# Kernel tuning notes

Hardware: AMD Instinct MI355X
Metric: run time of the kernel (lower is better)

Reference implementation:

```python
import jax, jax.numpy as jnp
import numpy as np

HEADS = 4
DIM_K = 16
DIM_U = 1
EPS = 1e-5


def _rel_pos_idx(n):
    # torch: meshgrid(ij) -> stack -> '(i j) n'; rel = pos[None,:]-pos[:,None] + n-1
    ii, jj = np.meshgrid(np.arange(n), np.arange(n), indexing='ij')
    pos = np.stack([ii, jj]).reshape(2, -1).T  # (n*n, 2)
    rel = pos[None, :] - pos[:, None] + (n - 1)  # (N, N, 2)
    return rel[..., 0], rel[..., 1]


def _bn(t, gamma, beta):
    # BatchNorm2d in training mode: batch stats over (b, h, w), biased var
    mu = t.mean(axis=(0, 1, 2))
    var = t.var(axis=(0, 1, 2))
    return (t - mu) * jax.lax.rsqrt(var + EPS) * gamma + beta


def setup_inputs() -> dict:
    key = jax.random.key(0)
    ks = jax.random.split(key, 16)
    b, n, c = 8, 48, 128
    hk = DIM_K * HEADS          # 64
    v = 128 // HEADS            # 32 (dim_out // heads)
    rl = 2 * n - 1              # 95
    s = 0.02
    return {
        'x': jax.random.normal(ks[0], (b, n, n, c), jnp.float32),
        'cor': jax.random.normal(ks[1], (b, n, n, 2), jnp.float32),
        'Wq': jax.random.normal(ks[2], (hk, c), jnp.float32) * s,
        'Wk': jax.random.normal(ks[3], (DIM_K * DIM_U, c), jnp.float32) * s,
        'Wv': jax.random.normal(ks[4], (v * DIM_U, c), jnp.float32) * s,
        'Wce': jax.random.normal(ks[5], (hk, 2), jnp.float32) * s,
        'bce': jax.random.normal(ks[6], (hk,), jnp.float32) * s,
        'Wcc': jax.random.normal(ks[7], (hk, 128), jnp.float32) * s,
        'Wmp': jax.random.normal(ks[8], (128, hk), jnp.float32) * s,
        'bmp': jax.random.normal(ks[9], (128,), jnp.float32) * s,
        'gq': jnp.ones((hk,), jnp.float32),
        'bq': jnp.zeros((hk,), jnp.float32),
        'gv': jnp.ones((v * DIM_U,), jnp.float32),
        'bv': jnp.zeros((v * DIM_U,), jnp.float32),
        'rel_pos_emb': jax.random.normal(ks[10], (rl, rl, DIM_K, DIM_U), jnp.float32),
    }


def reference(x, cor, Wq, Wk, Wv, Wce, bce, Wcc, Wmp, bmp, gq, bq, gv, bv, rel_pos_emb):
    b, hh, ww, c = x.shape
    h, u, kd = HEADS, DIM_U, DIM_K
    vd = Wv.shape[0] // u
    N = hh * ww

    # frame reversal along batch
    x_rev = jnp.concatenate([x[b // 2:], x[:b // 2]], axis=0)

    # 1x1 convs as channel matmuls (channels-last)
    q = jnp.einsum('bhwc,oc->bhwo', x, Wq)
    k = jnp.einsum('bhwc,oc->bhwo', x_rev, Wk)
    v = jnp.einsum('bhwc,oc->bhwo', x_rev, Wv)

    Qn = _bn(q, gq, bq)
    Vn = _bn(v, gv, bv)

    Q = jnp.transpose(Qn.reshape(b, N, h, kd), (0, 2, 3, 1))       # b h k n
    K = jnp.transpose(k.reshape(b, N, u, kd), (0, 2, 3, 1))        # b u k m
    V = jnp.transpose(Vn.reshape(b, N, u, vd), (0, 2, 3, 1))       # b u v m

    K = jax.nn.softmax(K, axis=-1)
    lamc = jnp.einsum('bukm,buvm->bkv', K, V)
    Yc = jnp.einsum('bhkn,bkv->bhvn', Q, lamc)

    # relative position lambda (global branch)
    ni, mi = _rel_pos_idx(hh)
    emb = rel_pos_emb[ni, mi]                                      # n m k u
    lamp = jnp.einsum('nmku,buvm->bnkv', emb, V)
    Yp = jnp.einsum('bhkn,bnkv->bhvn', Q, lamp)

    Y = Yc + Yp                                                    # b h v n
    appearance = jnp.transpose(Y.reshape(b, h, vd, hh, ww), (0, 3, 4, 1, 2)).reshape(b, hh, ww, h * vd)

    cor_embed_ = jnp.einsum('bhwc,oc->bhwo', cor, Wce) + bce       # b hh ww (h k)
    cor_embed = jnp.transpose(cor_embed_.reshape(b, N, h, kd), (0, 2, 3, 1))  # b h k n
    crc = jnp.einsum('bhkn,bkv->bhvn', cor_embed, lamc)
    crp = jnp.einsum('bhkn,bnkv->bhvn', cor_embed, lamp)
    cor_reverse_ = jnp.transpose((crc + crp).reshape(b, h, vd, hh, ww), (0, 3, 4, 1, 2)).reshape(b, hh, ww, h * vd)
    cor_reverse = jnp.einsum('bhwc,oc->bhwo', cor_reverse_, Wcc)
    motion = jnp.einsum('bhwc,oc->bhwo', cor_reverse - cor_embed_, Wmp) + bmp
    return appearance, motion
```

## Files before the change

### kernel.cpp

```cpp
#include <hip/hip_runtime.h>
#include <math.h>

#define NNPOS 2304
#define ROWS  18432
#define NK    96

#define O_Q   0ul
#define O_K   1179648ul
#define O_V   1474560ul
#define O_ST  2064384ul
#define O_VP  2064704ul
#define O_QP  2457920ul
#define O_LC  4817216ul
#define O_CR  4821312ul
#define O_RT  6000960ul
#define O_WG  6148416ul
#define O_B2  6148672ul
#define O_WB  6148800ul
#define O_PT  6155968ul
#define O_PV  6164160ul
#define O_PE  6166208ul
#define O_WFB 6167232ul

typedef __bf16 bf16x8 __attribute__((ext_vector_type(8)));
typedef float  f32x4  __attribute__((ext_vector_type(4)));
typedef unsigned int u32;
struct __attribute__((packed, aligned(4))) bf16x8p { bf16x8 v; };

__global__ void k_fold(const float* __restrict__ Wcc, const float* __restrict__ Wce,
                       const float* __restrict__ Wmp, const float* __restrict__ bmp,
                       const float* __restrict__ bce, const float* __restrict__ Wq,
                       const float* __restrict__ Wk, const float* __restrict__ Wv,
                       float* __restrict__ ws) {
  const int t = threadIdx.x;
  const int g = blockIdx.x * 256 + t;
  const int o2 = g >> 7, c = g & 127;
  float acc = 0.f;
#pragma unroll 8
  for (int o = 0; o < 64; ++o) acc += Wmp[o2 * 64 + o] * Wcc[o * 128 + c];
  ((__bf16*)(ws + O_WFB))[o2 * 128 + c] = (__bf16)acc;
  if (blockIdx.x == 0 && t < 128) {
    float a0 = 0.f, a1 = 0.f, ab = 0.f;
#pragma unroll 8
    for (int o = 0; o < 64; ++o) {
      float w = Wmp[t * 64 + o];
      a0 += w * Wce[o * 2]; a1 += w * Wce[o * 2 + 1]; ab += w * bce[o];
    }
    ws[O_WG + t * 2] = a0; ws[O_WG + t * 2 + 1] = a1; ws[O_B2 + t] = bmp[t] - ab;
  }
  __bf16* wbp = (__bf16*)(ws + O_WB);
  if (g < 14336) {
    float w;
    if (g < 8192) w = Wq[g];
    else if (g < 10240) w = Wk[g - 8192];
    else w = Wv[g - 10240];
    wbp[g] = (__bf16)w;
  }
}

__global__ __launch_bounds__(256) void k_qkv(const float* __restrict__ x,
                                             float* __restrict__ ws) {
  const int t = threadIdx.x;
  const int wave = t >> 6, lane = t & 63;
  const int lr = lane & 15, quad = lane >> 4;
  const int r0 = blockIdx.x * 64 + wave * 16;
  const int b = r0 / NNPOS;
  const int n0 = r0 - b * NNPOS;
  const size_t outbase = (size_t)(((b + 4) & 7)) * NNPOS + n0;

  const __bf16* wb = (const __bf16*)(ws + O_WB);
  const float* xrow = x + (size_t)(r0 + lr) * 128;

  f32x4 acc[7];
#pragma unroll
  for (int i = 0; i < 7; ++i) acc[i] = (f32x4){0.f, 0.f, 0.f, 0.f};

#pragma unroll
  for (int ks = 0; ks < 4; ++ks) {
    const float* ap = xrow + ks * 32 + quad * 8;
    float4 a0 = *(const float4*)(ap);
    float4 a1 = *(const float4*)(ap + 4);
    bf16x8 af;
    af[0] = (__bf16)a0.x; af[1] = (__bf16)a0.y; af[2] = (__bf16)a0.z; af[3] = (__bf16)a0.w;
    af[4] = (__bf16)a1.x; af[5] = (__bf16)a1.y; af[6] = (__bf16)a1.z; af[7] = (__bf16)a1.w;
#pragma unroll
    for (int ct = 0; ct < 7; ++ct) {
      bf16x8 bfrag = *(const bf16x8*)(wb + (ct * 16 + lr) * 128 + ks * 32 + quad * 8);
      acc[ct] = __builtin_amdgcn_mfma_f32_16x16x32_bf16(af, bfrag, acc[ct], 0, 0, 0);
    }
  }

#pragma unroll
  for (int ct = 0; ct < 7; ++ct) {
#pragma unroll
    for (int reg = 0; reg < 4; ++reg) {
      int m = quad * 4 + reg;
      int oc = ct * 16 + lr;
      float vvv = acc[ct][reg];
      if (ct < 4)      ws[O_Q + (size_t)(r0 + m) * 64 + oc] = vvv;
      else if (ct < 5) ws[O_K + (outbase + m) * 16 + (oc - 64)] = vvv;
      else             ws[O_V + (outbase + m) * 32 + (oc - 80)] = vvv;
    }
  }
}

__global__ void k_rt(const float* __restrict__ rel, float* __restrict__ ws) {
  __bf16* rt = (__bf16*)(ws + O_RT);
  int i = blockIdx.x * 256 + threadIdx.x;
  if (i < 144400) {
    int kc = i & 15, rr = i >> 4;
    int ri = rr / 95, rj = rr - ri * 95;
    int d = ri * 96 + rj;
    __bf16 v = (__bf16)rel[i];
    rt[(size_t)kc * 9216 + d] = v;
    if (d > 0) rt[147456ul + (size_t)kc * 9216 + d - 1] = v;
  }
}

__global__ void k_zero(float* __restrict__ ws) {
  __bf16* vp = (__bf16*)(ws + O_VP);
  int i = blockIdx.x * 256 + threadIdx.x;
  if (i < 4096) ws[O_LC + i] = 0.f;
  int bv = i / 96, rem = i - bv * 96;
  int mi = rem >> 1, h8 = rem & 1;
  uint4 z; z.x = 0; z.y = 0; z.z = 0; z.w = 0;
  *(uint4*)(vp + (size_t)bv * 3072 + mi * 64 + 48 + h8 * 8) = z;
}

__global__ void k_stats1(float* __restrict__ ws) {
  const int t = threadIdx.x, blk = blockIdx.x;
  __shared__ float sh[512];
  if (blk < 64) {
    const int ch = t & 63, rsub = t >> 6;
    const float* src = ws + O_Q;
    const int r0 = blk * 288;
    float s = 0.f, s2 = 0.f;
#pragma unroll 4
    for (int i = 0; i < 72; ++i) {
      float v = src[(size_t)(r0 + rsub + i * 4) * 64 + ch];
      s += v; s2 += v * v;
    }
    sh[t] = s; sh[256 + t] = s2;
    __syncthreads();
    if (t < 64) {
      float S = sh[t] + sh[t + 64] + sh[t + 128] + sh[t + 192];
      float S2 = sh[256 + t] + sh[256 + t + 64] + sh[256 + t + 128] + sh[256 + t + 192];
      ws[O_PT + blk * 128 + t * 2] = S; ws[O_PT + blk * 128 + t * 2 + 1] = S2;
    }
  } else if (blk < 96) {
    const int j = blk - 64;
    const int ch = t & 31, rsub = t >> 5;
    const float* src = ws + O_V;
    const int r0 = j * 576;
    float s = 0.f, s2 = 0.f;
#pragma unroll 4
    for (int i = 0; i < 72; ++i) {
      float v = src[(size_t)(r0 + rsub + i * 8) * 32 + ch];
      s += v; s2 += v * v;
    }
    sh[t] = s; sh[256 + t] = s2;
    __syncthreads();
    if (t < 32) {
      float S = 0.f, S2 = 0.f;
#pragma unroll
      for (int k = 0; k < 8; ++k) { S += sh[t + k * 32]; S2 += sh[256 + t + k * 32]; }
      ws[O_PV + j * 64 + t * 2] = S; ws[O_PV + j * 64 + t * 2 + 1] = S2;
    }
  } else {
    const int idx = blk - 96;
    const int b = idx >> 3, sl = idx & 7;
    const int kc = t & 15, rsub = t >> 4;
    const int r0 = b * 2304 + sl * 288;
    float s = 0.f;
#pragma unroll 2
    for (int i = 0; i < 18; ++i)
      s += __expf(ws[O_K + (size_t)(r0 + rsub + i * 16) * 16 + kc]);
    sh[t] = s;
    __syncthreads();
    if (t < 16) {
      float S = 0.f;
#pragma unroll
      for (int k = 0; k < 16; ++k) S += sh[t + k * 16];
      ws[O_PE + b * 128 + sl * 16 + t] = S;
    }
  }
}

__global__ void k_stats2(const float* __restrict__ gq, const float* __restrict__ bq,
                         const float* __restrict__ gv, const float* __restrict__ bv,
                         float* __restrict__ ws) {
  const int t = threadIdx.x;
  if (t < 64) {
    float S = 0.f, S2 = 0.f;
    for (int i = 0; i < 64; ++i) { S += ws[O_PT + i * 128 + t * 2]; S2 += ws[O_PT + i * 128 + t * 2 + 1]; }
    float mu = S / 18432.f, var = S2 / 18432.f - mu * mu;
    float sc = gq[t] * rsqrtf(var + 1e-5f);
    ws[O_ST + t] = sc; ws[O_ST + 64 + t] = bq[t] - mu * sc;
  } else if (t < 96) {
    int ch = t - 64;
    float S = 0.f, S2 = 0.f;
    for (int i = 0; i < 32; ++i) { S += ws[O_PV + i * 64 + ch * 2]; S2 += ws[O_PV + i * 64 + ch * 2 + 1]; }
    float mu = S / 18432.f, var = S2 / 18432.f - mu * mu;
    float sc = gv[ch] * rsqrtf(var + 1e-5f);
    ws[O_ST + 128 + ch] = sc; ws[O_ST + 160 + ch] = bv[ch] - mu * sc;
  } else if (t < 224) {
    int idx = t - 96; int b = idx >> 4, kc = idx & 15;
    float S = 0.f;
#pragma unroll
    for (int sl = 0; sl < 8; ++sl) S += ws[O_PE + b * 128 + sl * 16 + kc];
    ws[O_ST + 192 + idx] = 1.f / S;
  }
}

__global__ void k_vp(float* __restrict__ ws) {
  const int b = blockIdx.x / 48, mi = blockIdx.x - b * 48;
  const int t = threadIdx.x;
  __shared__ float Vn[48 * 33];
  const float* st = ws + O_ST;
  const int r0 = b * 2304 + mi * 48;
#pragma unroll
  for (int i = t; i < 1536; i += 256) {
    int r = i >> 5, j = i & 31;
    Vn[r * 33 + j] = ws[O_V + (size_t)(r0 + r) * 32 + j] * st[128 + j] + st[160 + j];
  }
  __syncthreads();
  __bf16* vp = (__bf16*)(ws + O_VP);
  const int j = t >> 3, seg = t & 7;
  unsigned short u[6];
#pragma unroll
  for (int q = 0; q < 6; ++q)
    u[q] = __builtin_bit_cast(unsigned short, (__bf16)Vn[(seg * 6 + q) * 33 + j]);
  u32 w0 = (u32)u[0] | ((u32)u[1] << 16);
  u32 w1 = (u32)u[2] | ((u32)u[3] << 16);
  u32 w2 = (u32)u[4] | ((u32)u[5] << 16);
  u32* dst = (u32*)(vp + (size_t)(b * 32 + j) * 3072 + mi * 64 + seg * 6);
  dst[0] = w0; dst[1] = w1; dst[2] = w2;
}

__global__ void k_prep(const float* __restrict__ cor, const float* __restrict__ Wce,
                       const float* __restrict__ bce, float* __restrict__ ws) {
  const int t = threadIdx.x;
  const int rl = t >> 5, j = t & 31;
  const int rid = blockIdx.x * 8 + rl;
  const int b = rid / NNPOS, n = rid - b * NNPOS;
  const float* st = ws + O_ST;
  float c0 = cor[rid * 2], c1 = cor[rid * 2 + 1];
#pragma unroll
  for (int ch = j; ch < 64; ch += 32) {
    float qn = ws[O_Q + (size_t)rid * 64 + ch] * st[ch] + st[64 + ch];
    ws[O_QP + (size_t)(n * 8 + b) * 128 + ch] = qn;
    float ce = c0 * Wce[ch * 2] + c1 * Wce[ch * 2 + 1] + bce[ch];
    ws[O_QP + (size_t)(n * 8 + b) * 128 + 64 + ch] = ce;
  }
}

__global__ void k_lamc(float* __restrict__ ws) {
  const int b = blockIdx.x / 36, sl = blockIdx.x - b * 36;
  const int t = threadIdx.x;
  __shared__ float eK[16][16];
  __shared__ float Vn[16][33];
  const float* st = ws + O_ST;
  const int kc = t & 15, vp_ = t >> 4;
  const int v0 = vp_ * 2, v1 = v0 + 1;
  float a0 = 0.f, a1 = 0.f;
  const int m0 = b * 2304 + sl * 64;
  const int jj = t & 31, rw = t >> 5;
  const float scj = st[128 + jj], bij = st[160 + jj];
  for (int ch = 0; ch < 4; ++ch) {
    const int mbase = m0 + ch * 16;
    eK[t >> 4][t & 15] = __expf(ws[O_K + (size_t)(mbase + (t >> 4)) * 16 + (t & 15)]);
    Vn[rw][jj]     = ws[O_V + (size_t)(mbase + rw) * 32 + jj] * scj + bij;
    Vn[rw + 8][jj] = ws[O_V + (size_t)(mbase + rw + 8) * 32 + jj] * scj + bij;
    __syncthreads();
#pragma unroll
    for (int m = 0; m < 16; ++m) {
      float e = eK[m][kc];
      a0 += e * Vn[m][v0];
      a1 += e * Vn[m][v1];
    }
    __syncthreads();
  }
  atomicAdd(&ws[O_LC + (size_t)(b * 16 + kc) * 32 + v0], a0);
  atomicAdd(&ws[O_LC + (size_t)(b * 16 + kc) * 32 + v1], a1);
}

__global__ __launch_bounds__(128, 3) void k_lamp(float* __restrict__ ws,
                                                 float* __restrict__ out) {
  __shared__ __align__(16) char smem[17408];
  bf16x8* Bs16 = (bf16x8*)smem;
  float* Cs = (float*)smem;

  const int t = threadIdx.x;
  const int bx = blockIdx.x;
  const int ni = bx / 6;
  const int sset = bx - ni * 6;
  const int s0 = (sset < 3) ? sset * 16 : (sset - 3) * 16 + 1;
  const int by = blockIdx.y;
  const int colbase = by * 64;
  const int w = t >> 6, lane = t & 63;
  const int lr = lane & 15, quad = lane >> 4;

  const __bf16* vp = (const __bf16*)(ws + O_VP);
  const __bf16* rtb = (const __bf16*)(ws + O_RT);

  const int u0 = t, u1 = t + 128;
  const int c0 = u0 >> 2, p0 = ((u0 & 3) - (c0 >> 1)) & 3;
  const int c1 = u1 >> 2, p1 = ((u1 & 3) - (c1 >> 1)) & 3;
  const __bf16* gB0 = vp + (size_t)(colbase + c0) * 3072 + p0 * 8;
  const __bf16* gB1 = vp + (size_t)(colbase + c1) * 3072 + p1 * 8;

  const int parity = (s0 + 1) & 1;
  const __bf16* baseA = rtb + (size_t)parity * 147456 +
                        (size_t)lr * 9216 + quad * 8 - 2 * (w * 4);

  f32x4 acc[4][4];
  {
    f32x4 zz = {0.f, 0.f, 0.f, 0.f};
#pragma unroll
    for (int i = 0; i < 4; ++i)
#pragma unroll
      for (int j = 0; j < 4; ++j) acc[i][j] = zz;
  }

  bf16x8 afA[4], afB[4], vb0, vb1;

  auto loadA = [&](int ksn, bf16x8* dst) {
    int mi = ksn >> 1, mj0 = (ksn & 1) << 5;
    const __bf16* p = baseA + (96 * (mi - ni + 47) + mj0 - s0 + 47 - parity);
#pragma unroll
    for (int rt = 0; rt < 4; ++rt)
      dst[rt] = ((const bf16x8p*)(p - 2 * rt))->v;
  };
  auto loadB = [&](int ksn) {
    int k0 = ksn * 32;
    vb0 = *(const bf16x8*)(gB0 + k0);
    vb1 = *(const bf16x8*)(gB1 + k0);
  };

  loadB(0);
  Bs16[u0] = vb0; Bs16[u1] = vb1;
  loadA(0, afA);
  loadB(1);
  __syncthreads();

  for (int ks = 0; ks < NK; ks += 2) {
    Bs16[256 + u0] = vb0; Bs16[256 + u1] = vb1;
    loadB(ks + 2 < NK ? ks + 2 : NK - 1);
    loadA(ks + 1, afB);
#pragma unroll
    for (int ct = 0; ct < 4; ++ct) {
      int col = ct * 16 + lr;
      bf16x8 bfr = Bs16[col * 4 + ((quad + (col >> 1)) & 3)];
#pragma unroll
      for (int rt = 0; rt < 4; ++rt)
        acc[rt][ct] = __builtin_amdgcn_mfma_f32_16x16x32_bf16(afA[rt], bfr, acc[rt][ct], 0, 0, 0);
    }
    __syncthreads();
    Bs16[u0] = vb0; Bs16[u1] = vb1;
    loadB(ks + 3 < NK ? ks + 3 : NK - 1);
    if (ks + 2 < NK) loadA(ks + 2, afA);
#pragma unroll
    for (int ct = 0; ct < 4; ++ct) {
      int col = ct * 16 + lr;
      bf16x8 bfr = Bs16[256 + col * 4 + ((quad + (col >> 1)) & 3)];
#pragma unroll
      for (int rt = 0; rt < 4; ++rt)
        acc[rt][ct] = __builtin_amdgcn_mfma_f32_16x16x32_bf16(afB[rt], bfr, acc[rt][ct], 0, 0, 0);
    }
    __syncthreads();
  }

  const float* lamcp = ws + O_LC;
  const float* Qp = ws + O_QP;
  __bf16* CRb = (__bf16*)(ws + O_CR);
  const int s = t >> 5, vv = t & 31;

  for (int h = 0; h < 2; ++h) {
    __syncthreads();
    if (w == h) {
#pragma unroll
      for (int rt = 0; rt < 4; ++rt) {
#pragma unroll
        for (int ct = 0; ct < 4; ++ct) {
          int col = ct * 16 + lr;
          int bb = by * 2 + (col >> 5);
          int vl = col & 31;
#pragma unroll
          for (int reg = 0; reg < 4; ++reg) {
            int row = rt * 16 + quad * 4 + reg;
            int kc = row & 15;
            float dinv = ws[O_ST + 192 + bb * 16 + kc];
            Cs[row * 68 + col] = acc[rt][ct][reg] + lamcp[(bb * 16 + kc) * 32 + vl] * dinv;
          }
        }
      }
    }
    __syncthreads();
#pragma unroll
    for (int i = 0; i < 16; ++i) {
      int combo = s * 16 + i;
      int hp = combo & 7, bl = (combo >> 3) & 1, nr = combo >> 4;
      int n = ni * 48 + s0 + 2 * (h * 4 + nr);
      int bb = by * 2 + bl;
      const float* qrow = Qp + ((size_t)(n * 8 + bb) * 8 + hp) * 16;
      const float* crow = Cs + (nr * 16) * 68 + bl * 32 + vv;
      float y = 0.f;
#pragma unroll
      for (int kc = 0; kc < 16; ++kc) y += qrow[kc] * crow[kc * 68];
      size_t idx = (size_t)(bb * NNPOS + n) * 128 + (hp & 3) * 32 + vv;
      if (hp < 4) out[idx] = y;
      else        CRb[idx] = (__bf16)y;
    }
  }
}

__global__ __launch_bounds__(256) void k_motion(const float* __restrict__ cor,
                                                float* __restrict__ ws,
                                                float* __restrict__ out) {
  const int t = threadIdx.x;
  const int wave = t >> 6, lane = t & 63;
  const int lr = lane & 15, quad = lane >> 4;
  const int r0 = blockIdx.x * 64 + wave * 16;
  const __bf16* crb = (const __bf16*)(ws + O_CR);
  const __bf16* wfb = (const __bf16*)(ws + O_WFB);

  f32x4 acc[8];
#pragma unroll
  for (int i = 0; i < 8; ++i) acc[i] = (f32x4){0.f, 0.f, 0.f, 0.f};

#pragma unroll
  for (int ks = 0; ks < 4; ++ks) {
    bf16x8 af = *(const bf16x8*)(crb + (size_t)(r0 + lr) * 128 + ks * 32 + quad * 8);
#pragma unroll
    for (int ct = 0; ct < 8; ++ct) {
      bf16x8 bfrag = *(const bf16x8*)(wfb + (ct * 16 + lr) * 128 + ks * 32 + quad * 8);
      acc[ct] = __builtin_amdgcn_mfma_f32_16x16x32_bf16(af, bfrag, acc[ct], 0, 0, 0);
    }
  }

#pragma unroll
  for (int reg = 0; reg < 4; ++reg) {
    int row = r0 + quad * 4 + reg;
    float c0 = cor[row * 2], c1 = cor[row * 2 + 1];
#pragma unroll
    for (int ct = 0; ct < 8; ++ct) {
      int o2 = ct * 16 + lr;
      float y = acc[ct][reg] + ws[O_B2 + o2] - c0 * ws[O_WG + o2 * 2] - c1 * ws[O_WG + o2 * 2 + 1];
      out[2359296ul + (size_t)row * 128 + o2] = y;
    }
  }
}

extern "C" void kernel_launch(void* const* d_in, const int* in_sizes, int n_in,
                              void* d_out, int out_size, void* d_ws, size_t ws_size,
                              hipStream_t stream) {
  const float* x   = (const float*)d_in[0];
  const float* cor = (const float*)d_in[1];
  const float* Wq  = (const float*)d_in[2];
  const float* Wk  = (const float*)d_in[3];
  const float* Wv  = (const float*)d_in[4];
  const float* Wce = (const float*)d_in[5];
  const float* bce = (const float*)d_in[6];
  const float* Wcc = (const float*)d_in[7];
  const float* Wmp = (const float*)d_in[8];
  const float* bmp = (const float*)d_in[9];
  const float* gq  = (const float*)d_in[10];
  const float* bq  = (const float*)d_in[11];
  const float* gv  = (const float*)d_in[12];
  const float* bv  = (const float*)d_in[13];
  const float* rel = (const float*)d_in[14];
  float* out = (float*)d_out;
  float* ws  = (float*)d_ws;

  k_fold  <<<64, 256, 0, stream>>>(Wcc, Wce, Wmp, bmp, bce, Wq, Wk, Wv, ws);
  k_qkv   <<<288, 256, 0, stream>>>(x, ws);
  k_rt    <<<565, 256, 0, stream>>>(rel, ws);
  k_zero  <<<96, 256, 0, stream>>>(ws);
  k_stats1<<<160, 256, 0, stream>>>(ws);
  k_stats2<<<1, 256, 0, stream>>>(gq, bq, gv, bv, ws);
  k_vp    <<<384, 256, 0, stream>>>(ws);
  k_lamc  <<<288, 256, 0, stream>>>(ws);
  k_prep  <<<2304, 256, 0, stream>>>(cor, Wce, bce, ws);
  k_lamp  <<<dim3(288, 4), 128, 0, stream>>>(ws, out);
  k_motion<<<288, 256, 0, stream>>>(cor, ws, out);
}
```

Before: 298.5 us.

## Stage relative-position A operand in LDS and widen lamp tiles to 128 columns

The k_lamp GEMM now runs with 256-thread blocks over 128 output columns, so the grid's y dimension drops from 4 to 2. Each block gathers the relative-position embedding window into LDS once per k-step as packed u32 and shares it across waves, instead of every wave doing unaligned global loads of A. The B operand is streamed with global_load_lds double buffering, and the duplicate parity-shifted copy of the embedding table in k_rt is removed. The aim is less redundant global traffic for A and better reuse per block. The cost is more LDS per block, a sync every k-step, lower occupancy, and scalar handling of odd-aligned gathers.

```diff
diff --git a/kernel.cpp b/kernel.cpp
--- a/kernel.cpp
+++ b/kernel.cpp
@@ -1,5 +1,6 @@
 #include <hip/hip_runtime.h>
 #include <math.h>
+#include <stdint.h>
 
 #define NNPOS 2304
 #define ROWS  18432
@@ -25,7 +26,13 @@
 typedef __bf16 bf16x8 __attribute__((ext_vector_type(8)));
 typedef float  f32x4  __attribute__((ext_vector_type(4)));
 typedef unsigned int u32;
-struct __attribute__((packed, aligned(4))) bf16x8p { bf16x8 v; };
+typedef u32 u32x4 __attribute__((ext_vector_type(4)));
+
+__device__ __forceinline__ void gll16(const void* g, void* l) {
+  auto gp = (const __attribute__((address_space(1))) unsigned char*)(uintptr_t)g;
+  auto lp = (__attribute__((address_space(3))) unsigned char*)(u32)(uintptr_t)l;
+  __builtin_amdgcn_global_load_lds(gp, lp, 16, 0, 0);
+}
 
 __global__ void k_fold(const float* __restrict__ Wcc, const float* __restrict__ Wce,
                        const float* __restrict__ Wmp, const float* __restrict__ bmp,
@@ -110,10 +117,7 @@
   if (i < 144400) {
     int kc = i & 15, rr = i >> 4;
     int ri = rr / 95, rj = rr - ri * 95;
-    int d = ri * 96 + rj;
-    __bf16 v = (__bf16)rel[i];
-    rt[(size_t)kc * 9216 + d] = v;
-    if (d > 0) rt[147456ul + (size_t)kc * 9216 + d - 1] = v;
+    rt[(size_t)kc * 9216 + ri * 96 + rj] = (__bf16)rel[i];
   }
 }
 
@@ -284,10 +288,11 @@
   atomicAdd(&ws[O_LC + (size_t)(b * 16 + kc) * 32 + v1], a1);
 }
 
-__global__ __launch_bounds__(128, 3) void k_lamp(float* __restrict__ ws,
+__global__ __launch_bounds__(256, 2) void k_lamp(float* __restrict__ ws,
                                                  float* __restrict__ out) {
-  __shared__ __align__(16) char smem[17408];
+  __shared__ __align__(16) char smem[33792];
   bf16x8* Bs16 = (bf16x8*)smem;
+  u32* Sw = (u32*)(smem + 16384);
   float* Cs = (float*)smem;
 
   const int t = threadIdx.x;
@@ -295,23 +300,40 @@
   const int ni = bx / 6;
   const int sset = bx - ni * 6;
   const int s0 = (sset < 3) ? sset * 16 : (sset - 3) * 16 + 1;
-  const int by = blockIdx.y;
-  const int colbase = by * 64;
+  const int chalf = blockIdx.y;
+  const int colbase = chalf * 128;
   const int w = t >> 6, lane = t & 63;
+  const int wrow = w >> 1, wcol = w & 1;
   const int lr = lane & 15, quad = lane >> 4;
 
   const __bf16* vp = (const __bf16*)(ws + O_VP);
-  const __bf16* rtb = (const __bf16*)(ws + O_RT);
-
-  const int u0 = t, u1 = t + 128;
-  const int c0 = u0 >> 2, p0 = ((u0 & 3) - (c0 >> 1)) & 3;
-  const int c1 = u1 >> 2, p1 = ((u1 & 3) - (c1 >> 1)) & 3;
-  const __bf16* gB0 = vp + (size_t)(colbase + c0) * 3072 + p0 * 8;
-  const __bf16* gB1 = vp + (size_t)(colbase + c1) * 3072 + p1 * 8;
-
-  const int parity = (s0 + 1) & 1;
-  const __bf16* baseA = rtb + (size_t)parity * 147456 +
-                        (size_t)lr * 9216 + quad * 8 - 2 * (w * 4);
+  const unsigned short* rp = (const unsigned short*)(ws + O_RT);
+
+  const int kcA0 = t / 24, wpA0 = t - kcA0 * 24;
+  const int ia1 = t + 256;
+  const int kcA1 = ia1 / 24, wpA1 = ia1 - kcA1 * 24;
+  const bool hasA1 = (t < 128);
+
+  const int u0 = w * 64 + lane, u1 = 256 + w * 64 + lane;
+  const int cB0 = u0 >> 2, pB0 = ((u0 & 3) - ((u0 >> 3) & 3)) & 3;
+  const int cB1 = u1 >> 2, pB1 = ((u1 & 3) - ((u1 >> 3) & 3)) & 3;
+  const __bf16* gB0 = vp + (size_t)(colbase + cB0) * 3072 + pB0 * 8;
+  const __bf16* gB1 = vp + (size_t)(colbase + cB1) * 3072 + pB1 * 8;
+  char* ldsB0 = smem + w * 1024;
+  char* ldsB1 = smem + 4096 + w * 1024;
+
+  auto gatherA = [&](int ksn, u32& a0_, u32& a1_) {
+    const int mi = ksn >> 1, mj0 = (ksn & 1) << 5;
+    const int P0 = 96 * (mi - ni + 47) + mj0 - s0 + 33;
+    long b0 = (long)kcA0 * 9216 + P0 + 2 * wpA0;
+    if (P0 & 1) a0_ = (u32)rp[b0] | ((u32)rp[b0 + 1] << 16);
+    else        a0_ = *(const u32*)(rp + b0);
+    if (hasA1) {
+      long b1 = (long)kcA1 * 9216 + P0 + 2 * wpA1;
+      if (P0 & 1) a1_ = (u32)rp[b1] | ((u32)rp[b1 + 1] << 16);
+      else        a1_ = *(const u32*)(rp + b1);
+    }
+  };
 
   f32x4 acc[4][4];
   {
@@ -322,51 +344,47 @@
       for (int j = 0; j < 4; ++j) acc[i][j] = zz;
   }
 
-  bf16x8 afA[4], afB[4], vb0, vb1;
-
-  auto loadA = [&](int ksn, bf16x8* dst) {
-    int mi = ksn >> 1, mj0 = (ksn & 1) << 5;
-    const __bf16* p = baseA + (96 * (mi - ni + 47) + mj0 - s0 + 47 - parity);
+  u32 a0 = 0, a1 = 0;
+  {
+    u32 p0, p1 = 0;
+    gatherA(0, p0, p1);
+    Sw[kcA0 * 25 + wpA0] = p0;
+    if (hasA1) Sw[kcA1 * 25 + wpA1] = p1;
+    gll16(gB0, ldsB0);
+    gll16(gB1, ldsB1);
+    gatherA(1, a0, a1);
+  }
+  __syncthreads();
+
+  for (int ks = 0; ks < NK; ++ks) {
+    const int cur = ks & 1, nxt = cur ^ 1;
+    if (ks + 1 < NK) {
+      const int k0n = (ks + 1) * 32;
+      gll16(gB0 + k0n, ldsB0 + nxt * 8192);
+      gll16(gB1 + k0n, ldsB1 + nxt * 8192);
+      Sw[nxt * 400 + kcA0 * 25 + wpA0] = a0;
+      if (hasA1) Sw[nxt * 400 + kcA1 * 25 + wpA1] = a1;
+    }
+    if (ks + 2 < NK) gatherA(ks + 2, a0, a1);
+
+    bf16x8 af[4], bfr[4];
+#pragma unroll
+    for (int rt = 0; rt < 4; ++rt) {
+      int nl = wrow * 4 + rt;
+      int wb = cur * 400 + lr * 25 + (7 - nl) + quad * 4;
+      u32x4 dd = { Sw[wb], Sw[wb + 1], Sw[wb + 2], Sw[wb + 3] };
+      af[rt] = __builtin_bit_cast(bf16x8, dd);
+    }
+#pragma unroll
+    for (int ct = 0; ct < 4; ++ct) {
+      int col = wcol * 64 + ct * 16 + lr;
+      bfr[ct] = Bs16[cur * 512 + col * 4 + ((quad + (col >> 1)) & 3)];
+    }
 #pragma unroll
     for (int rt = 0; rt < 4; ++rt)
-      dst[rt] = ((const bf16x8p*)(p - 2 * rt))->v;
-  };
-  auto loadB = [&](int ksn) {
-    int k0 = ksn * 32;
-    vb0 = *(const bf16x8*)(gB0 + k0);
-    vb1 = *(const bf16x8*)(gB1 + k0);
-  };
-
-  loadB(0);
-  Bs16[u0] = vb0; Bs16[u1] = vb1;
-  loadA(0, afA);
-  loadB(1);
-  __syncthreads();
-
-  for (int ks = 0; ks < NK; ks += 2) {
-    Bs16[256 + u0] = vb0; Bs16[256 + u1] = vb1;
-    loadB(ks + 2 < NK ? ks + 2 : NK - 1);
-    loadA(ks + 1, afB);
-#pragma unroll
-    for (int ct = 0; ct < 4; ++ct) {
-      int col = ct * 16 + lr;
-      bf16x8 bfr = Bs16[col * 4 + ((quad + (col >> 1)) & 3)];
-#pragma unroll
-      for (int rt = 0; rt < 4; ++rt)
-        acc[rt][ct] = __builtin_amdgcn_mfma_f32_16x16x32_bf16(afA[rt], bfr, acc[rt][ct], 0, 0, 0);
-    }
-    __syncthreads();
-    Bs16[u0] = vb0; Bs16[u1] = vb1;
-    loadB(ks + 3 < NK ? ks + 3 : NK - 1);
-    if (ks + 2 < NK) loadA(ks + 2, afA);
-#pragma unroll
-    for (int ct = 0; ct < 4; ++ct) {
-      int col = ct * 16 + lr;
-      bf16x8 bfr = Bs16[256 + col * 4 + ((quad + (col >> 1)) & 3)];
-#pragma unroll
-      for (int rt = 0; rt < 4; ++rt)
-        acc[rt][ct] = __builtin_amdgcn_mfma_f32_16x16x32_bf16(afB[rt], bfr, acc[rt][ct], 0, 0, 0);
-    }
+#pragma unroll
+      for (int ct = 0; ct < 4; ++ct)
+        acc[rt][ct] = __builtin_amdgcn_mfma_f32_16x16x32_bf16(af[rt], bfr[ct], acc[rt][ct], 0, 0, 0);
     __syncthreads();
   }
 
@@ -377,20 +395,20 @@
 
   for (int h = 0; h < 2; ++h) {
     __syncthreads();
-    if (w == h) {
+    if (wrow == h) {
 #pragma unroll
       for (int rt = 0; rt < 4; ++rt) {
 #pragma unroll
         for (int ct = 0; ct < 4; ++ct) {
-          int col = ct * 16 + lr;
-          int bb = by * 2 + (col >> 5);
+          int col = wcol * 64 + ct * 16 + lr;
+          int bb = chalf * 4 + (col >> 5);
           int vl = col & 31;
 #pragma unroll
           for (int reg = 0; reg < 4; ++reg) {
             int row = rt * 16 + quad * 4 + reg;
             int kc = row & 15;
             float dinv = ws[O_ST + 192 + bb * 16 + kc];
-            Cs[row * 68 + col] = acc[rt][ct][reg] + lamcp[(bb * 16 + kc) * 32 + vl] * dinv;
+            Cs[row * 132 + col] = acc[rt][ct][reg] + lamcp[(bb * 16 + kc) * 32 + vl] * dinv;
           }
         }
       }
@@ -399,14 +417,14 @@
 #pragma unroll
     for (int i = 0; i < 16; ++i) {
       int combo = s * 16 + i;
-      int hp = combo & 7, bl = (combo >> 3) & 1, nr = combo >> 4;
+      int hp = combo & 7, bl = (combo >> 3) & 3, nr = combo >> 5;
       int n = ni * 48 + s0 + 2 * (h * 4 + nr);
-      int bb = by * 2 + bl;
+      int bb = chalf * 4 + bl;
       const float* qrow = Qp + ((size_t)(n * 8 + bb) * 8 + hp) * 16;
-      const float* crow = Cs + (nr * 16) * 68 + bl * 32 + vv;
+      const float* crow = Cs + (nr * 16) * 132 + bl * 32 + vv;
       float y = 0.f;
 #pragma unroll
-      for (int kc = 0; kc < 16; ++kc) y += qrow[kc] * crow[kc * 68];
+      for (int kc = 0; kc < 16; ++kc) y += qrow[kc] * crow[kc * 132];
       size_t idx = (size_t)(bb * NNPOS + n) * 128 + (hp & 3) * 32 + vv;
       if (hp < 4) out[idx] = y;
       else        CRb[idx] = (__bf16)y;
@@ -481,6 +499,6 @@
   k_vp    <<<384, 256, 0, stream>>>(ws);
   k_lamc  <<<288, 256, 0, stream>>>(ws);
   k_prep  <<<2304, 256, 0, stream>>>(cor, Wce, bce, ws);
-  k_lamp  <<<dim3(288, 4), 128, 0, stream>>>(ws, out);
+  k_lamp  <<<dim3(288, 2), 256, 0, stream>>>(ws, out);
   k_motion<<<288, 256, 0, stream>>>(cor, ws, out);
 }
```

New measurement: 268.0 us. 10.2% less time.
